# Performance work log

Hardware: AMD Instinct MI355X
Metric: run time of the kernel (lower is better)

Reference implementation:

```python
import jax, jax.numpy as jnp
from jax import lax
import numpy as np


def conv2d(x, w, b=None, stride=1, pad=0, groups=1):
    out = lax.conv_general_dilated(x, w, (stride, stride), [(pad, pad), (pad, pad)],
                                   dimension_numbers=('NCHW', 'OIHW', 'NCHW'),
                                   feature_group_count=groups)
    if b is not None:
        out = out + b[None, :, None, None]
    return out


def ln(x, g, b, eps=1e-5):
    m = x.mean(-1, keepdims=True)
    v = ((x - m) ** 2).mean(-1, keepdims=True)
    return (x - m) * lax.rsqrt(v + eps) * g + b


def grid_sample_bilinear(img, grid):
    # img [N,C,H,W]; grid [N,Hg,Wg,2] with (x,y) in [-1,1]; align_corners=True, zeros padding
    N, C, H, W = img.shape
    x = (grid[..., 0] + 1.0) * 0.5 * (W - 1)
    y = (grid[..., 1] + 1.0) * 0.5 * (H - 1)
    x0 = jnp.floor(x); y0 = jnp.floor(y)
    x1 = x0 + 1.0; y1 = y0 + 1.0
    wx1 = x - x0; wx0 = 1.0 - wx1
    wy1 = y - y0; wy0 = 1.0 - wy1
    imgh = img.transpose(0, 2, 3, 1)  # [N,H,W,C]
    bidx = jnp.arange(N)[:, None, None]
    def g(ix, iy):
        valid = (ix >= 0) & (ix <= W - 1) & (iy >= 0) & (iy <= H - 1)
        ixc = jnp.clip(ix, 0, W - 1).astype(jnp.int32)
        iyc = jnp.clip(iy, 0, H - 1).astype(jnp.int32)
        return imgh[bidx, iyc, ixc] * valid[..., None].astype(img.dtype)
    out = (g(x0, y0) * (wx0 * wy0)[..., None] + g(x1, y0) * (wx1 * wy0)[..., None]
           + g(x0, y1) * (wx0 * wy1)[..., None] + g(x1, y1) * (wx1 * wy1)[..., None])
    return out.transpose(0, 3, 1, 2)  # [N,C,Hg,Wg]


def setup_inputs() -> dict:
    key = jax.random.key(0)
    ks = iter(jax.random.split(key, 64))
    def rn(shape, s=0.02):
        return jax.random.normal(next(ks), shape, jnp.float32) * s
    B, C, H, W = 4, 512, 32, 32
    gc, hid = 256, 1024
    d = {}
    d['feat_tgt'] = jax.random.normal(next(ks), (B, C, H, W), jnp.float32)
    d['feat_ref'] = jax.random.normal(next(ks), (B, C, H, W), jnp.float32)
    d['emb_w'] = rn((C, 2 * C, 3, 3)); d['emb_b'] = jnp.zeros((C,), jnp.float32)
    d['q_w'] = rn((C, C)); d['q_b'] = jnp.zeros((C,), jnp.float32)
    d['k_w'] = rn((C, C)); d['k_b'] = jnp.zeros((C,), jnp.float32)
    d['v_w'] = rn((C, C)); d['v_b'] = jnp.zeros((C,), jnp.float32)
    d['out_w'] = rn((C, C)); d['out_b'] = jnp.zeros((C,), jnp.float32)
    d['ln1_w'] = jnp.ones((gc,), jnp.float32); d['ln1_b'] = jnp.zeros((gc,), jnp.float32)
    d['mb_n1_w'] = jnp.ones((gc,), jnp.float32); d['mb_n1_b'] = jnp.zeros((gc,), jnp.float32)
    d['mb_q_w'] = rn((gc, gc)); d['mb_q_b'] = jnp.zeros((gc,), jnp.float32)
    d['mb_kv_w'] = rn((2 * gc, gc)); d['mb_kv_b'] = jnp.zeros((2 * gc,), jnp.float32)
    d['mb_proj_w'] = rn((gc, gc)); d['mb_proj_b'] = jnp.zeros((gc,), jnp.float32)
    d['mb_n2_w'] = jnp.ones((gc,), jnp.float32); d['mb_n2_b'] = jnp.zeros((gc,), jnp.float32)
    d['mb_fc1_w'] = rn((hid, gc)); d['mb_fc1_b'] = jnp.zeros((hid,), jnp.float32)
    d['mb_dw_w'] = rn((hid, 1, 3, 3)); d['mb_dw_b'] = jnp.zeros((hid,), jnp.float32)
    d['mb_fc2_w'] = rn((gc, hid)); d['mb_fc2_b'] = jnp.zeros((gc,), jnp.float32)
    d['co_dw_w'] = rn((gc, 1, 9, 9)); d['co_dw_b'] = jnp.zeros((gc,), jnp.float32)
    d['co_ln_w'] = jnp.ones((gc,), jnp.float32); d['co_ln_b'] = jnp.zeros((gc,), jnp.float32)
    d['co_out_w'] = rn((2, gc))
    return d


def reference(feat_tgt, feat_ref, emb_w, emb_b, q_w, q_b, k_w, k_b, v_w, v_b, out_w, out_b,
              ln1_w, ln1_b, mb_n1_w, mb_n1_b, mb_q_w, mb_q_b, mb_kv_w, mb_kv_b,
              mb_proj_w, mb_proj_b, mb_n2_w, mb_n2_b, mb_fc1_w, mb_fc1_b, mb_dw_w, mb_dw_b,
              mb_fc2_w, mb_fc2_b, co_dw_w, co_dw_b, co_ln_w, co_ln_b, co_out_w):
    B, C, H, W = feat_tgt.shape
    G = 2                      # n_groups
    gc = C // G                # n_group_channels
    heads, hc = 8, C // 8      # n_heads, n_head_channels
    # embedding conv over concat(target, reference)
    feat = conv2d(jnp.concatenate([feat_tgt, feat_ref], 1), emb_w, emb_b, pad=1)
    q = jnp.einsum('bchw,oc->bohw', feat_tgt, q_w) + q_b[None, :, None, None]
    # group tokens + LN
    fg = feat.reshape(B * G, gc, H * W).transpose(0, 2, 1)  # [BG, N, gc]
    x = ln(fg, ln1_w, ln1_b)
    # ---- MitBlock offset generator ----
    BG, N, D = x.shape
    mh = 8; mhd = D // mh
    h = ln(x, mb_n1_w, mb_n1_b, 1e-6)
    qq = (h @ mb_q_w.T + mb_q_b).reshape(BG, N, mh, mhd).transpose(0, 2, 1, 3)
    kv = (h @ mb_kv_w.T + mb_kv_b).reshape(BG, N, 2, mh, mhd).transpose(2, 0, 3, 1, 4)
    kk, vv = kv[0], kv[1]
    a = jax.nn.softmax(jnp.einsum('bhnd,bhmd->bhnm', qq, kk) * (mhd ** -0.5), axis=-1)
    o = jnp.einsum('bhnm,bhmd->bhnd', a, vv).transpose(0, 2, 1, 3).reshape(BG, N, D)
    x = x + (o @ mb_proj_w.T + mb_proj_b)
    h2 = ln(x, mb_n2_w, mb_n2_b, 1e-6)
    m = h2 @ mb_fc1_w.T + mb_fc1_b                         # [BG, N, hid]
    hid = m.shape[-1]
    mi = m.transpose(0, 2, 1).reshape(BG, hid, H, W)
    mi = conv2d(mi, mb_dw_w, mb_dw_b, pad=1, groups=hid)
    m = jax.nn.gelu(mi.reshape(BG, hid, N).transpose(0, 2, 1), approximate=False)
    x = x + (m @ mb_fc2_w.T + mb_fc2_b)
    # ---- conv_offset stack ----
    off = x.reshape(BG, H, W, gc).transpose(0, 3, 1, 2)
    off = conv2d(off, co_dw_w, co_dw_b, pad=4, groups=gc)
    off = ln(off.transpose(0, 2, 3, 1), co_ln_w, co_ln_b).transpose(0, 3, 1, 2)
    off = jax.nn.gelu(off, approximate=False)
    off = jnp.einsum('bchw,oc->bohw', off, co_out_w)       # [BG, 2, Hk, Wk]
    Hk, Wk = off.shape[2], off.shape[3]
    ns = Hk * Wk
    rng = jnp.array([1.0 / Hk, 1.0 / Wk], feat.dtype).reshape(1, 2, 1, 1)
    off = jnp.tanh(off) * rng * 2.0                        # offset_range_factor = 2
    off = off.transpose(0, 2, 3, 1)                        # [BG, Hk, Wk, 2] (y,x)
    ry = (jnp.linspace(0.5, Hk - 0.5, Hk, dtype=feat.dtype) / Hk) * 2 - 1
    rx = (jnp.linspace(0.5, Wk - 0.5, Wk, dtype=feat.dtype) / Wk) * 2 - 1
    ref = jnp.stack(jnp.meshgrid(ry, rx, indexing='ij'), -1)  # [Hk, Wk, 2] (y,x)
    pos = off + ref[None]
    sampled = grid_sample_bilinear(feat.reshape(BG, gc, H, W), pos[..., ::-1])
    sampled = sampled.reshape(B, C, ns)
    k = jnp.einsum('bcn,oc->bon', sampled, k_w) + k_b[None, :, None]
    v = jnp.einsum('bcn,oc->bon', sampled, v_w) + v_b[None, :, None]
    qh = q.reshape(B * heads, hc, H * W)
    kh = k.reshape(B * heads, hc, ns)
    vh = v.reshape(B * heads, hc, ns)
    attn = jax.nn.softmax(jnp.einsum('bcm,bcn->bmn', qh, kh) * (hc ** -0.5), axis=-1)
    out = jnp.einsum('bmn,bcn->bcm', attn, vh).reshape(B, C, H, W)
    y = jnp.einsum('bchw,oc->bohw', out, out_w) + out_b[None, :, None, None]
    return y
```

## Files before the change

### kernel.cpp

```cpp
#include <hip/hip_runtime.h>
#include <math.h>


static constexpr int HW = 1024;

typedef __attribute__((ext_vector_type(8))) short bf16x8;
typedef __attribute__((ext_vector_type(4))) float f32x4;

union V16u { int4 i4; ushort u[8]; };

__device__ __forceinline__ float gelu_exact(float v) {
  return 0.5f * v * (1.0f + erff(v * 0.7071067811865475f));
}

__device__ __forceinline__ ushort bf16_rne(float v) {
  unsigned int b = __float_as_uint(v);
  return (ushort)((b + 0x7fffu + ((b >> 16) & 1u)) >> 16);
}

__device__ __forceinline__ void split2(float v, ushort& h, ushort& l) {
  h = bf16_rne(v);
  l = bf16_rne(v - __uint_as_float(((unsigned int)h) << 16));
}

__global__ void k_prepw(const float* __restrict__ w, ushort* __restrict__ Wt_hi,
                        ushort* __restrict__ Wt_lo) {
  int idx = blockIdx.x * 256 + threadIdx.x;
  int o = idx >> 10, ci = idx & 1023;
  const float* src = w + (size_t)idx * 9;
#pragma unroll
  for (int t = 0; t < 9; ++t) {
    ushort h, l; split2(src[t], h, l);
    size_t oo = ((size_t)(t * 512 + o)) * 1024 + ci;
    Wt_hi[oo] = h; Wt_lo[oo] = l;
  }
}

__global__ void k_prepx(const float* __restrict__ tgt, const float* __restrict__ refp,
                        ushort* __restrict__ Xt_hi, ushort* __restrict__ Xt_lo) {
  int idx = blockIdx.x * 256 + threadIdx.x;
  int xp = idx % 34; int r = idx / 34;
  int g8 = r & 127; r >>= 7;
  int yp = r % 34; int b = r / 34;
  int y = yp - 1, x = xp - 1;
  bool valid = (unsigned)y < 32u && (unsigned)x < 32u;
  V16u hi, lo;
  const float* in = (g8 < 64) ? (tgt + ((size_t)(b * 512 + g8 * 8)) * HW)
                              : (refp + ((size_t)(b * 512 + (g8 - 64) * 8)) * HW);
#pragma unroll
  for (int j = 0; j < 8; ++j) {
    float v = valid ? in[(size_t)j * HW + y * 32 + x] : 0.f;
    split2(v, hi.u[j], lo.u[j]);
  }
  size_t oo = (((size_t)(b * 34 + yp)) * 34 + xp) * 1024 + g8 * 8;
  *(int4*)(Xt_hi + oo) = hi.i4;
  *(int4*)(Xt_lo + oo) = lo.i4;
}

__global__ __launch_bounds__(256, 2)
void k_emb_mfma(const ushort* __restrict__ Xt_hi, const ushort* __restrict__ Xt_lo,
                const ushort* __restrict__ Wt_hi, const ushort* __restrict__ Wt_lo,
                float* __restrict__ part) {
  int wgid = (blockIdx.x & 7) * 64 + (blockIdx.x >> 3);
  int yt = wgid & 7;  wgid >>= 3;
  int b  = wgid & 3;  wgid >>= 2;
  int mt = wgid & 3;  wgid >>= 2;
  int ks = wgid;
  int tid = threadIdx.x;
  int w = tid >> 6, l = tid & 63;
  int lr = l & 15, lu = l >> 4;
  int y0 = yt * 4;
  int obase = mt * 128 + w * 32;

  __shared__ int4 LsH[2][816];
  __shared__ int4 LsL[2][816];

  int4 gh[4], gl[4];
  int kc0 = ks * 8;

  auto loadstage = [&](int kcg) {
#pragma unroll
    for (int i = 0; i < 4; ++i) {
      int s = tid + 256 * i;
      if (s < 816) {
        int px = s >> 2;
        int u = (s & 3) ^ ((px >> 1) & 3);
        size_t off = ((size_t)(b * 34 + y0) * 34 + px) * 1024 + kcg * 32 + u * 8;
        gh[i] = *(const int4*)(Xt_hi + off);
        gl[i] = *(const int4*)(Xt_lo + off);
// ... 65 lines not shown
  for (int a = 0; a < 2; ++a)
#pragma unroll
    for (int yr = 0; yr < 4; ++yr)
#pragma unroll
      for (int h = 0; h < 2; ++h) {
        f32x4 c = acc[a][yr * 2 + h];
        size_t base = ((size_t)(b * 512 + obase + a * 16 + lu * 4)) * 1024
                      + (y0 + yr) * 32 + h * 16 + lr;
#pragma unroll
        for (int r = 0; r < 4; ++r) pb[base + (size_t)r * 1024] = c[r];
      }
}

__global__ void k_embmerge_nc(const float* __restrict__ part, const float* __restrict__ bias,
                              float* __restrict__ featnc) {
  __shared__ float T[64][65];
  int bid = blockIdx.x;
  int n0 = (bid & 15) << 6; bid >>= 4;
  int c0 = (bid & 3) << 6; int bg = bid >> 2;
  int cl = threadIdx.x & 63, rw = threadIdx.x >> 6;
#pragma unroll
  for (int i = 0; i < 16; ++i) {
    int crow = i * 4 + rw;
    size_t idx = ((size_t)(bg * 256 + c0 + crow)) * 1024 + n0 + cl;
    float v = part[idx] + part[2097152 + idx] + part[4194304 + idx] + part[6291456 + idx];
    T[crow][cl] = v + bias[(bg & 1) * 256 + c0 + crow];
  }
  __syncthreads();
#pragma unroll
  for (int i = 0; i < 16; ++i) {
    int nrow = i * 4 + rw;
    featnc[((size_t)(bg * 1024 + n0 + nrow)) * 256 + c0 + cl] = T[cl][nrow];
  }
}

__device__ __forceinline__ void wfrag_body(const float* __restrict__ W, int K, int KC,
                                           ushort* __restrict__ dh, ushort* __restrict__ dl,
                                           int gtid) {
  int l = gtid & 63; int fr = gtid >> 6;
  int kc = fr % KC; int ot = fr / KC;
  int lr = l & 15, lu = l >> 4;
  const float* sp = W + (size_t)(ot * 16 + lr) * K + kc * 32 + lu * 8;
  V16u hi, lo;
#pragma unroll
  for (int j = 0; j < 8; ++j) split2(sp[j], hi.u[j], lo.u[j]);
  *(int4*)(dh + (size_t)gtid * 8) = hi.i4;
  *(int4*)(dl + (size_t)gtid * 8) = lo.i4;
}

__global__ void k_prep_wfrag9(
    const float* q_w, const float* k_w, const float* v_w, const float* o_w,
    const float* mq_w, const float* mkv_w, const float* mp_w,
    const float* f1_w, const float* f2_w, const float* dw9_w,
    ushort* qh, ushort* ql, ushort* kh, ushort* kl, ushort* vh, ushort* vl,
    ushort* oh, ushort* ol, ushort* mqh, ushort* mql, ushort* mkvh, ushort* mkvl,
    ushort* mph, ushort* mpl, ushort* f1h, ushort* f1l, ushort* f2h, ushort* f2l,
    float* wt9) {
  int bid = blockIdx.x, tid = threadIdx.x;
  if (bid < 128)      wfrag_body(q_w, 512, 16, qh, ql, bid * 256 + tid);
  else if (bid < 256) wfrag_body(k_w, 512, 16, kh, kl, (bid - 128) * 256 + tid);
  else if (bid < 384) wfrag_body(v_w, 512, 16, vh, vl, (bid - 256) * 256 + tid);
  else if (bid < 512) wfrag_body(o_w, 512, 16, oh, ol, (bid - 384) * 256 + tid);
  else if (bid < 544) wfrag_body(mq_w, 256, 8, mqh, mql, (bid - 512) * 256 + tid);
  else if (bid < 608) wfrag_body(mkv_w, 256, 8, mkvh, mkvl, (bid - 544) * 256 + tid);
  else if (bid < 640) wfrag_body(mp_w, 256, 8, mph, mpl, (bid - 608) * 256 + tid);
  else if (bid < 768) wfrag_body(f1_w, 256, 8, f1h, f1l, (bid - 640) * 256 + tid);
  else if (bid < 896) wfrag_body(f2_w, 1024, 32, f2h, f2l, (bid - 768) * 256 + tid);
  else {
    int idx = (bid - 896) * 256 + tid;
    int t = idx >> 8, c = idx & 255;
    wt9[idx] = dw9_w[c * 81 + t];
  }
}

__global__ void k_prep_cm2frag(const float* __restrict__ src, int CH, int KC,
                               ushort* __restrict__ dh, ushort* __restrict__ dl) {
  int gtid = blockIdx.x * 256 + threadIdx.x;
  int l = gtid & 63; int fr = gtid >> 6;
  int kc = fr % KC; int r2 = fr / KC; int nt = r2 & 63; int b = r2 >> 6;
  int lr = l & 15, lu = l >> 4;
  const float* sp = src + ((size_t)(b * CH) + kc * 32 + lu * 8) * 1024 + nt * 16 + lr;
  V16u hi, lo;
#pragma unroll
  for (int j = 0; j < 8; ++j) split2(sp[(size_t)j * 1024], hi.u[j], lo.u[j]);
  *(int4*)(dh + (size_t)gtid * 8) = hi.i4;
  *(int4*)(dl + (size_t)gtid * 8) = lo.i4;
}

__global__ void k_prep_s2frag(const float* __restrict__ snc,
                              ushort* __restrict__ dh, ushort* __restrict__ dl) {
  int gtid = blockIdx.x * 256 + threadIdx.x;
  int l = gtid & 63; int fr = gtid >> 6;
  int kc = fr & 15; int nt = (fr >> 4) & 63; int b = fr >> 10;
  int lr = l & 15, lu = l >> 4;
  const float* sp = snc + ((size_t)((b * 2 + (kc >> 3)) * 1024 + nt * 16 + lr)) * 256
                    + (kc & 7) * 32 + lu * 8;
  V16u hi, lo;
#pragma unroll
  for (int j = 0; j < 8; ++j) split2(sp[j], hi.u[j], lo.u[j]);
  *(int4*)(dh + (size_t)gtid * 8) = hi.i4;
  *(int4*)(dl + (size_t)gtid * 8) = lo.i4;
}

__global__ __launch_bounds__(256)
void k_gemm_mfma(const ushort* __restrict__ Ah, const ushort* __restrict__ Al,
                 const ushort* __restrict__ Bh, const ushort* __restrict__ Bl,
                 const float* __restrict__ bias, float* __restrict__ Y,
                 int KC, int MT, int Mtot) {
  int bid = blockIdx.x;
  int ntb = bid & 15; bid >>= 4;
  int mt = bid % MT; int b = bid / MT;
  int tid = threadIdx.x, w = tid >> 6, l = tid & 63, lr = l & 15, lu = l >> 4;
  int wo = w >> 1, wn = w & 1;
  int ot0 = mt * 4 + wo * 2;
  int nf0 = ntb * 4 + wn * 2;
  const bf16x8* pAh = (const bf16x8*)Ah;
  const bf16x8* pAl = (const bf16x8*)Al;
  const bf16x8* pBh = (const bf16x8*)Bh;
  const bf16x8* pBl = (const bf16x8*)Bl;
// ... 43 lines not shown
#pragma unroll
  for (int i = 0; i < 16; ++i) {
    int crow = i * 4 + rw;
    T[crow][cl] = Pcm[((size_t)(bg * 256 + c0 + crow)) * 1024 + n0 + cl];
  }
  __syncthreads();
#pragma unroll
  for (int i = 0; i < 16; ++i) {
    int nrow = i * 4 + rw;
    Xtm[((size_t)((bg << 10) + n0 + nrow)) * 256 + c0 + cl] += T[cl][nrow];
  }
}

__global__ void k_transadd_nc(const float* __restrict__ Yg, const float* __restrict__ Xtm,
                              float* __restrict__ out_nc) {
  __shared__ float T[64][65];
  int bid = blockIdx.x; int n0 = (bid & 15) << 6; bid >>= 4;
  int c0 = (bid & 3) << 6; int bg = bid >> 2;
  int cl = threadIdx.x & 63, rw = threadIdx.x >> 6;
#pragma unroll
  for (int i = 0; i < 16; ++i) {
    int crow = i * 4 + rw;
    T[crow][cl] = Yg[((size_t)(bg * 256 + c0 + crow)) * 1024 + n0 + cl];
  }
  __syncthreads();
#pragma unroll
  for (int i = 0; i < 16; ++i) {
    int nrow = i * 4 + rw;
    size_t a = ((size_t)((bg << 10) + n0 + nrow)) * 256 + c0 + cl;
    out_nc[a] = T[cl][nrow] + Xtm[a];
  }
}

__global__ void k_ln_tok(const float* __restrict__ xin, const float* __restrict__ g_,
                         const float* __restrict__ b_, float* __restrict__ yo, float eps) {
  int token = (blockIdx.x * 256 + threadIdx.x) >> 6;
  int lane = threadIdx.x & 63;
  float4 v4 = *reinterpret_cast<const float4*>(xin + (size_t)token * 256 + lane * 4);
  float s  = v4.x + v4.y + v4.z + v4.w;
  float s2 = v4.x * v4.x + v4.y * v4.y + v4.z * v4.z + v4.w * v4.w;
#pragma unroll
  for (int off = 32; off; off >>= 1) { s += __shfl_xor(s, off); s2 += __shfl_xor(s2, off); }
  float mean = s * (1.f / 256.f);
  float rstd = rsqrtf(s2 * (1.f / 256.f) - mean * mean + eps);
  float4 g4 = *reinterpret_cast<const float4*>(g_ + lane * 4);
  float4 b4 = *reinterpret_cast<const float4*>(b_ + lane * 4);
  float4 o;
  o.x = (v4.x - mean) * rstd * g4.x + b4.x;
  o.y = (v4.y - mean) * rstd * g4.y + b4.y;
  o.z = (v4.z - mean) * rstd * g4.z + b4.z;
  o.w = (v4.w - mean) * rstd * g4.w + b4.w;
  *reinterpret_cast<float4*>(yo + (size_t)token * 256 + lane * 4) = o;
}

__global__ void k_ln_frag(const float* __restrict__ xin, const float* __restrict__ g_,
                          const float* __restrict__ b_, ushort* __restrict__ dh,
                          ushort* __restrict__ dl, float eps) {
  int token = (blockIdx.x * 256 + threadIdx.x) >> 6;
  int lane = threadIdx.x & 63;
  float4 v4 = *reinterpret_cast<const float4*>(xin + (size_t)token * 256 + lane * 4);
  float s  = v4.x + v4.y + v4.z + v4.w;
  float s2 = v4.x * v4.x + v4.y * v4.y + v4.z * v4.z + v4.w * v4.w;
#pragma unroll
  for (int off = 32; off; off >>= 1) { s += __shfl_xor(s, off); s2 += __shfl_xor(s2, off); }
  float mean = s * (1.f / 256.f);
  float rstd = rsqrtf(s2 * (1.f / 256.f) - mean * mean + eps);
  float4 g4 = *reinterpret_cast<const float4*>(g_ + lane * 4);
  float4 b4 = *reinterpret_cast<const float4*>(b_ + lane * 4);
  float vals[4];
  vals[0] = (v4.x - mean) * rstd * g4.x + b4.x;
  vals[1] = (v4.y - mean) * rstd * g4.y + b4.y;
  vals[2] = (v4.z - mean) * rstd * g4.z + b4.z;
  vals[3] = (v4.w - mean) * rstd * g4.w + b4.w;
  ushort4 h4, l4;
  split2(vals[0], h4.x, l4.x); split2(vals[1], h4.y, l4.y);
  split2(vals[2], h4.z, l4.z); split2(vals[3], h4.w, l4.w);
  int bg = token >> 10, nt = (token >> 4) & 63, lr = token & 15;
  int kc = lane >> 3, lu_f = (lane >> 1) & 3, j0 = (lane & 1) * 4;
  size_t base = ((((size_t)(bg * 64 + nt)) * 8 + kc) * 64 + lu_f * 16 + lr) * 8 + j0;
  *(ushort4*)(dh + base) = h4;
  *(ushort4*)(dl + base) = l4;
}

__global__ void k_prep_mb3(const float* __restrict__ qq_cm, const float* __restrict__ kv_cm,
                           ushort* __restrict__ mQh, ushort* __restrict__ mQl,
                           ushort* __restrict__ mKh, ushort* __restrict__ mKl,
                           ushort* __restrict__ mVh, ushort* __restrict__ mVl) {
  int bid = blockIdx.x, tid = threadIdx.x;
  int sect = bid >> 10, lb = bid & 1023;
  int gtid = lb * 256 + tid;
  int l = gtid & 63; int fr = gtid >> 6;
  int lr = l & 15, lu = l >> 4;
  V16u hi, lo;
  if (sect < 2) {
    int nt = fr & 63; int bgh = fr >> 6;
    int bg = bgh >> 3, hh = bgh & 7;
    const float* src = sect == 0 ? qq_cm : kv_cm;
    int CH = sect == 0 ? 256 : 512;
    float scale = sect == 0 ? 0.17677669529663689f : 1.f;
    const float* sp = src + ((size_t)(bg * CH + hh * 32 + lu * 8)) * 1024 + nt * 16 + lr;
#pragma unroll
    for (int j = 0; j < 8; ++j) split2(sp[(size_t)j * 1024] * scale, hi.u[j], lo.u[j]);
    ushort* dh = sect == 0 ? mQh : mKh;
    ushort* dl = sect == 0 ? mQl : mKl;
    *(int4*)(dh + (size_t)gtid * 8) = hi.i4;
    *(int4*)(dl + (size_t)gtid * 8) = lo.i4;
  } else {
    int kc = fr & 31; int et = (fr >> 5) & 1; int bgh = fr >> 6;
    int bg = bgh >> 3, hh = bgh & 7;
    const float* sp = kv_cm + ((size_t)(bg * 512 + 256 + hh * 32 + et * 16 + lr)) * 1024
                      + kc * 32 + lu * 8;
#pragma unroll
    for (int j = 0; j < 8; ++j) split2(sp[j], hi.u[j], lo.u[j]);
    *(int4*)(mVh + (size_t)gtid * 8) = hi.i4;
    *(int4*)(mVl + (size_t)gtid * 8) = lo.i4;
  }
}

__global__ void k_prep_main3(const float* __restrict__ qb, const float* __restrict__ kb,
                             const float* __restrict__ vb,
                             ushort* __restrict__ aQh, ushort* __restrict__ aQl,
                             ushort* __restrict__ aKh, ushort* __restrict__ aKl,
                             ushort* __restrict__ aVh, ushort* __restrict__ aVl) {
  int bid = blockIdx.x, tid = threadIdx.x;
  int sect = bid >> 10, lb = bid & 1023;
  int gtid = lb * 256 + tid;
  int l = gtid & 63, tile = gtid >> 6;
  int lr = l & 15, lu = l >> 4;
  V16u hi, lo;
  if (sect < 2) {
    int dc = tile & 1, nt = (tile >> 1) & 63, bh = tile >> 7;
    int b = bh >> 3, h = bh & 7;
    const float* src = sect == 0 ? qb : kb;
    float scale = sect == 0 ? 0.125f : 1.f;
    const float* sp = src + ((size_t)(b * 512 + h * 64 + dc * 32 + lu * 8)) * 1024
                      + nt * 16 + lr;
#pragma unroll
    for (int j = 0; j < 8; ++j) split2(sp[(size_t)j * 1024] * scale, hi.u[j], lo.u[j]);
    ushort* dh = sect == 0 ? aQh : aKh;
    ushort* dl = sect == 0 ? aQl : aKl;
    *(int4*)(dh + (size_t)gtid * 8) = hi.i4;
    *(int4*)(dl + (size_t)gtid * 8) = lo.i4;
  } else {
    int kc = tile & 31, et = (tile >> 5) & 3, bh = tile >> 7;
    int b = bh >> 3, h = bh & 7;
    const float* sp = vb + ((size_t)(b * 512 + h * 64 + et * 16 + lr)) * 1024 + kc * 32 + lu * 8;
#pragma unroll
    for (int j = 0; j < 8; ++j) split2(sp[j], hi.u[j], lo.u[j]);
    *(int4*)(aVh + (size_t)gtid * 8) = hi.i4;
    *(int4*)(aVl + (size_t)gtid * 8) = lo.i4;
  }
}

__global__ __launch_bounds__(256)
void k_mbattn_mfma(const ushort* __restrict__ Qh, const ushort* __restrict__ Ql,
                   const ushort* __restrict__ Kh, const ushort* __restrict__ Kl,
                   const ushort* __restrict__ Vh, const ushort* __restrict__ Vl,
                   ushort* __restrict__ ofh, ushort* __restrict__ ofl) {
  int qb = blockIdx.x & 15, bgh = blockIdx.x >> 4;
  int tid = threadIdx.x, w = tid >> 6, l = tid & 63, lr = l & 15, lu = l >> 4;
  int qt = qb * 4 + w;
  bf16x8 qh = ((const bf16x8*)Qh)[(size_t)(bgh * 64 + qt) * 64 + l];
  bf16x8 ql = ((const bf16x8*)Ql)[(size_t)(bgh * 64 + qt) * 64 + l];
  __shared__ ushort Ph[4][16][72];
  __shared__ ushort Pl[4][16][72];
  f32x4 zero = {0.f, 0.f, 0.f, 0.f};
  f32x4 oacc[2] = {zero, zero};
  float den = 0.f;
  for (int kb = 0; kb < 16; ++kb) {
#pragma unroll
    for (int kt4 = 0; kt4 < 4; ++kt4) {
      int kt = kb * 4 + kt4;
      bf16x8 kh = ((const bf16x8*)Kh)[(size_t)(bgh * 64 + kt) * 64 + l];
      bf16x8 kl = ((const bf16x8*)Kl)[(size_t)(bgh * 64 + kt) * 64 + l];
      f32x4 s = zero;
      s = __builtin_amdgcn_mfma_f32_16x16x32_bf16(kh, qh, s, 0, 0, 0);
      s = __builtin_amdgcn_mfma_f32_16x16x32_bf16(kh, ql, s, 0, 0, 0);
      s = __builtin_amdgcn_mfma_f32_16x16x32_bf16(kl, qh, s, 0, 0, 0);
      uint2 uh, ul;
// ... 265 lines not shown
  const float* n1_b   = (const float*)d_in[15];
  const float* mbq_w  = (const float*)d_in[16];
  const float* mbq_b  = (const float*)d_in[17];
  const float* mbkv_w = (const float*)d_in[18];
  const float* mbkv_b = (const float*)d_in[19];
  const float* mbp_w  = (const float*)d_in[20];
  const float* mbp_b  = (const float*)d_in[21];
  const float* n2_w   = (const float*)d_in[22];
  const float* n2_b   = (const float*)d_in[23];
  const float* fc1_w  = (const float*)d_in[24];
  const float* fc1_b  = (const float*)d_in[25];
  const float* dw3_w  = (const float*)d_in[26];
  const float* dw3_b  = (const float*)d_in[27];
  const float* fc2_w  = (const float*)d_in[28];
  const float* fc2_b  = (const float*)d_in[29];
  const float* dw9_w  = (const float*)d_in[30];
  const float* dw9_b  = (const float*)d_in[31];
  const float* coln_w = (const float*)d_in[32];
  const float* coln_b = (const float*)d_in[33];
  const float* coout_w= (const float*)d_in[34];

  float* ws = (float*)d_ws;
  float* slabA = ws + 0;
  float* qbuf  = ws + 2097152;
  float* xbuf  = ws + 4194304;
  float* slabD = ws + 6291456;
  float* slabE = ws + 8388608;
  float* slabF = ws + 10485760;
  float* slabG = ws + 14680064;
  float* slabH = ws + 23068672;
  float* featnc= ws + 31457280;
  float* posb  = ws + 35389440;
  float* wt9   = ws + 35405824;

  ushort* XtH = (ushort*)(ws + 4194304);
  ushort* XtL = XtH + 4734976;
  ushort* WtEH = (ushort*)slabG;
  ushort* WtEL = WtEH + 4718592;
  float* part = slabH;
  ushort* tgtfh = (ushort*)slabF;
  ushort* tgtfl = tgtfh + 2097152;

  ushort* J = (ushort*)(ws + 33554432);
  ushort* wfq_h = J;                ushort* wfq_l = J + 262144;
  ushort* wfk_h = J + 524288;       ushort* wfk_l = J + 786432;
  ushort* wfv_h = J + 1048576;      ushort* wfv_l = J + 1310720;
  ushort* wfo_h = J + 1572864;      ushort* wfo_l = J + 1835008;
  ushort* wfmq_h = J + 2097152;     ushort* wfmq_l = J + 2162688;
  ushort* wfmkv_h = J + 2228224;    ushort* wfmkv_l = J + 2359296;
  ushort* wfmp_h = J + 2490368;     ushort* wfmp_l = J + 2555904;
  ushort* wff1_h = J + 2621440;     ushort* wff1_l = J + 2883584;
  ushort* wff2_h = J + 3145728;     ushort* wff2_l = J + 3407872;

  ushort* hfh = (ushort*)slabG;     ushort* hfl = hfh + 2097152;
  float* qq_cm  = slabE;
  float* kv_cm  = slabF;
  ushort* mQh = (ushort*)slabG;     ushort* mQl = mQh + 2097152;
  ushort* mKh = mQh + 4194304;      ushort* mKl = mQh + 6291456;
  ushort* mVh = mQh + 8388608;      ushort* mVl = mQh + 10485760;
  ushort* ofh = (ushort*)slabF;     ushort* ofl = ofh + 2097152;
  float* P_cm = slabD;
  ushort* h2fh = (ushort*)slabF;    ushort* h2fl = h2fh + 2097152;
  float* m_cm = slabG;
  float* mi_cm = slabH;
  ushort* mifh = (ushort*)slabG;    ushort* mifl = mifh + 8388608;
  float* ygemm = slabD;
  float* offin = slabA;
  float* offdwnc = slabE;
  float* samplednc = slabA;
  ushort* sfh = (ushort*)slabF;     ushort* sfl = sfh + 2097152;
  float* kbuf = slabD;
  float* vbuf = slabE;
  ushort* aQh = (ushort*)slabG;     ushort* aQl = aQh + 2097152;
  ushort* aKh = aQh + 4194304;      ushort* aKl = aQh + 6291456;
  ushort* aVh = aQh + 8388608;      ushort* aVl = aQh + 10485760;
  ushort* anfh = (ushort*)slabH;    ushort* anfl = anfh + 2097152;

  k_prepw<<<2048, 256, 0, stream>>>(emb_w, WtEH, WtEL);
  k_prepx<<<2312, 256, 0, stream>>>(tgt, refp, XtH, XtL);
  k_prep_wfrag9<<<977, 256, 0, stream>>>(q_w, k_w, v_w, out_w, mbq_w, mbkv_w, mbp_w,
                                         fc1_w, fc2_w, dw9_w,
                                         wfq_h, wfq_l, wfk_h, wfk_l, wfv_h, wfv_l,
                                         wfo_h, wfo_l, wfmq_h, wfmq_l, wfmkv_h, wfmkv_l,
                                         wfmp_h, wfmp_l, wff1_h, wff1_l, wff2_h, wff2_l,
                                         wt9);
  k_prep_cm2frag<<<1024, 256, 0, stream>>>(tgt, 512, 16, tgtfh, tgtfl);
  k_emb_mfma<<<512, 256, 0, stream>>>(XtH, XtL, WtEH, WtEL, part);
  k_embmerge_nc<<<512, 256, 0, stream>>>(part, emb_b, featnc);
  k_gemm_mfma<<<512, 256, 0, stream>>>(wfq_h, wfq_l, tgtfh, tgtfl, q_b, qbuf, 16, 8, 512);
  k_ln_tok<<<2048, 256, 0, stream>>>(featnc, ln1_w, ln1_b, xbuf, 1e-5f);
  k_ln_frag<<<2048, 256, 0, stream>>>(xbuf, n1_w, n1_b, hfh, hfl, 1e-6f);
  k_gemm_mfma<<<512, 256, 0, stream>>>(wfmq_h, wfmq_l, hfh, hfl, mbq_b, qq_cm, 8, 4, 256);
  k_gemm_mfma<<<1024, 256, 0, stream>>>(wfmkv_h, wfmkv_l, hfh, hfl, mbkv_b, kv_cm, 8, 8, 512);
  k_prep_mb3<<<3072, 256, 0, stream>>>(qq_cm, kv_cm, mQh, mQl, mKh, mKl, mVh, mVl);
  k_mbattn_mfma<<<1024, 256, 0, stream>>>(mQh, mQl, mKh, mKl, mVh, mVl, ofh, ofl);
  k_gemm_mfma<<<512, 256, 0, stream>>>(wfmp_h, wfmp_l, ofh, ofl, mbp_b, P_cm, 8, 4, 256);
  k_transadd_tm<<<512, 256, 0, stream>>>(P_cm, xbuf);
  k_ln_frag<<<2048, 256, 0, stream>>>(xbuf, n2_w, n2_b, h2fh, h2fl, 1e-6f);
  k_gemm_mfma<<<2048, 256, 0, stream>>>(wff1_h, wff1_l, h2fh, h2fl, fc1_b, m_cm, 8, 16, 1024);
  k_dw3<<<32768, 256, 0, stream>>>(m_cm, dw3_w, dw3_b, mi_cm);
  k_prep_cm2frag<<<4096, 256, 0, stream>>>(mi_cm, 1024, 32, mifh, mifl);
  k_gemm_mfma<<<512, 256, 0, stream>>>(wff2_h, wff2_l, mifh, mifl, fc2_b, ygemm, 32, 4, 256);
  k_transadd_nc<<<512, 256, 0, stream>>>(ygemm, xbuf, offin);
  k_dw9_nc<<<1024, 256, 0, stream>>>(offin, wt9, dw9_b, offdwnc);
  k_cotail_nc<<<2048, 256, 0, stream>>>(offdwnc, coln_w, coln_b, coout_w, posb);
  k_gsample_nc<<<128, 256, 0, stream>>>(featnc, posb, samplednc);
  k_prep_s2frag<<<1024, 256, 0, stream>>>(samplednc, sfh, sfl);
  k_gemm_mfma<<<512, 256, 0, stream>>>(wfk_h, wfk_l, sfh, sfl, k_b, kbuf, 16, 8, 512);
  k_gemm_mfma<<<512, 256, 0, stream>>>(wfv_h, wfv_l, sfh, sfl, v_b, vbuf, 16, 8, 512);
  k_prep_main3<<<3072, 256, 0, stream>>>(qbuf, kbuf, vbuf, aQh, aQl, aKh, aKl, aVh, aVl);
  k_mainattn_mfma<<<512, 256, 0, stream>>>(aQh, aQl, aKh, aKl, aVh, aVl, anfh, anfl);
  k_gemm_mfma<<<512, 256, 0, stream>>>(wfo_h, wfo_l, anfh, anfl, out_b, (float*)d_out, 16, 8, 512);
}
```

Measured before the change: 619.2 us.

## Merge prep kernels, fuse both layernorms, and concatenate QKV and KV projection GEMMs

Folds the three weight/input prep launches into one kernel, which also concatenates biases. Fuses LN1 and the n1 norm into one kernel that writes both the fp32 token buffer and the bf16 hi/lo fragments. Merges the separate q/kv projections (mixer) and k/v projections (main attention) into single wider GEMMs over concatenated weights. The aim is fewer launches and fewer passes over the activation inputs, at the cost of new buffer layouts whose offsets must stay consistent.

Result: faster. 591.5 us (-4.5%).

```diff
diff --git a/kernel.cpp b/kernel.cpp
--- a/kernel.cpp
+++ b/kernel.cpp
@@ -23,38 +23,100 @@
   l = bf16_rne(v - __uint_as_float(((unsigned int)h) << 16));
 }
 
-__global__ void k_prepw(const float* __restrict__ w, ushort* __restrict__ Wt_hi,
-                        ushort* __restrict__ Wt_lo) {
-  int idx = blockIdx.x * 256 + threadIdx.x;
-  int o = idx >> 10, ci = idx & 1023;
-  const float* src = w + (size_t)idx * 9;
-#pragma unroll
-  for (int t = 0; t < 9; ++t) {
-    ushort h, l; split2(src[t], h, l);
-    size_t oo = ((size_t)(t * 512 + o)) * 1024 + ci;
-    Wt_hi[oo] = h; Wt_lo[oo] = l;
-  }
-}
-
-__global__ void k_prepx(const float* __restrict__ tgt, const float* __restrict__ refp,
-                        ushort* __restrict__ Xt_hi, ushort* __restrict__ Xt_lo) {
-  int idx = blockIdx.x * 256 + threadIdx.x;
-  int xp = idx % 34; int r = idx / 34;
-  int g8 = r & 127; r >>= 7;
-  int yp = r % 34; int b = r / 34;
-  int y = yp - 1, x = xp - 1;
-  bool valid = (unsigned)y < 32u && (unsigned)x < 32u;
+__device__ __forceinline__ void wfrag_body(const float* __restrict__ W, int K, int KC,
+                                           ushort* __restrict__ dh, ushort* __restrict__ dl,
+                                           int gtid) {
+  int l = gtid & 63; int fr = gtid >> 6;
+  int kc = fr % KC; int ot = fr / KC;
+  int lr = l & 15, lu = l >> 4;
+  const float* sp = W + (size_t)(ot * 16 + lr) * K + kc * 32 + lu * 8;
   V16u hi, lo;
-  const float* in = (g8 < 64) ? (tgt + ((size_t)(b * 512 + g8 * 8)) * HW)
-                              : (refp + ((size_t)(b * 512 + (g8 - 64) * 8)) * HW);
-#pragma unroll
-  for (int j = 0; j < 8; ++j) {
-    float v = valid ? in[(size_t)j * HW + y * 32 + x] : 0.f;
-    split2(v, hi.u[j], lo.u[j]);
-  }
-  size_t oo = (((size_t)(b * 34 + yp)) * 34 + xp) * 1024 + g8 * 8;
-  *(int4*)(Xt_hi + oo) = hi.i4;
-  *(int4*)(Xt_lo + oo) = lo.i4;
+#pragma unroll
+  for (int j = 0; j < 8; ++j) split2(sp[j], hi.u[j], lo.u[j]);
+  *(int4*)(dh + (size_t)gtid * 8) = hi.i4;
+  *(int4*)(dl + (size_t)gtid * 8) = lo.i4;
+}
+
+__global__ void k_prep_all(
+    const float* __restrict__ emb_w, const float* __restrict__ tgt,
+    const float* __restrict__ refp,
+    const float* q_w, const float* k_w, const float* v_w, const float* o_w,
+    const float* mq_w, const float* mkv_w, const float* mp_w,
+    const float* f1_w, const float* f2_w, const float* dw9_w,
+    const float* mq_b, const float* mkv_b, const float* k_b, const float* v_b,
+    ushort* __restrict__ WtEH, ushort* __restrict__ WtEL,
+    ushort* __restrict__ XtH, ushort* __restrict__ XtL,
+    ushort* qh, ushort* ql, ushort* kvh, ushort* kvl,
+    ushort* oh, ushort* ol, ushort* mqkvh, ushort* mqkvl,
+    ushort* mph, ushort* mpl, ushort* f1h, ushort* f1l, ushort* f2h, ushort* f2l,
+    float* wt9, float* biasmb, float* biaskv) {
+  int bid = blockIdx.x, tid = threadIdx.x;
+  if (bid < 2048) {
+    int idx = bid * 256 + tid;
+    int o = idx >> 10, ci = idx & 1023;
+    const float* src = emb_w + (size_t)idx * 9;
+#pragma unroll
+    for (int t = 0; t < 9; ++t) {
+      ushort h, l; split2(src[t], h, l);
+      size_t oo = ((size_t)(t * 512 + o)) * 1024 + ci;
+      WtEH[oo] = h; WtEL[oo] = l;
+    }
+  } else if (bid < 4360) {
+    int idx = (bid - 2048) * 256 + tid;
+    int xp = idx % 34; int r = idx / 34;
+    int g8 = r & 127; r >>= 7;
+    int yp = r % 34; int b = r / 34;
+    int y = yp - 1, x = xp - 1;
+    bool valid = (unsigned)y < 32u && (unsigned)x < 32u;
+    V16u hi, lo;
+    const float* in = (g8 < 64) ? (tgt + ((size_t)(b * 512 + g8 * 8)) * HW)
+                                : (refp + ((size_t)(b * 512 + (g8 - 64) * 8)) * HW);
+#pragma unroll
+    for (int j = 0; j < 8; ++j) {
+      float v = valid ? in[(size_t)j * HW + y * 32 + x] : 0.f;
+      split2(v, hi.u[j], lo.u[j]);
+    }
+    size_t oo = (((size_t)(b * 34 + yp)) * 34 + xp) * 1024 + g8 * 8;
+    *(int4*)(XtH + oo) = hi.i4;
+    *(int4*)(XtL + oo) = lo.i4;
+  }
+  else if (bid < 4488) wfrag_body(q_w, 512, 16, qh, ql, (bid - 4360) * 256 + tid);
+  else if (bid < 4616) wfrag_body(k_w, 512, 16, kvh, kvl, (bid - 4488) * 256 + tid);
+  else if (bid < 4744) wfrag_body(v_w, 512, 16, kvh + 262144, kvl + 262144,
+                                  (bid - 4616) * 256 + tid);
+  else if (bid < 4872) wfrag_body(o_w, 512, 16, oh, ol, (bid - 4744) * 256 + tid);
+  else if (bid < 4904) wfrag_body(mq_w, 256, 8, mqkvh, mqkvl, (bid - 4872) * 256 + tid);
+  else if (bid < 4968) wfrag_body(mkv_w, 256, 8, mqkvh + 65536, mqkvl + 65536,
+                                  (bid - 4904) * 256 + tid);
+  else if (bid < 5000) wfrag_body(mp_w, 256, 8, mph, mpl, (bid - 4968) * 256 + tid);
+  else if (bid < 5128) wfrag_body(f1_w, 256, 8, f1h, f1l, (bid - 5000) * 256 + tid);
+  else if (bid < 5256) wfrag_body(f2_w, 1024, 32, f2h, f2l, (bid - 5128) * 256 + tid);
+  else if (bid < 5337) {
+    int idx = (bid - 5256) * 256 + tid;
+    int t = idx >> 8, c = idx & 255;
+    wt9[idx] = dw9_w[c * 81 + t];
+  } else {
+    int idx = (bid - 5337) * 256 + tid;
+    if (idx < 768) biasmb[idx] = idx < 256 ? mq_b[idx] : mkv_b[idx - 256];
+    else if (idx < 1792) {
+      int j = idx - 768;
+      biaskv[j] = j < 512 ? k_b[j] : v_b[j - 512];
+    }
+  }
+}
+
+__global__ void k_prep_cm2frag(const float* __restrict__ src, int CH, int KC,
+                               ushort* __restrict__ dh, ushort* __restrict__ dl) {
+  int gtid = blockIdx.x * 256 + threadIdx.x;
+  int l = gtid & 63; int fr = gtid >> 6;
+  int kc = fr % KC; int r2 = fr / KC; int nt = r2 & 63; int b = r2 >> 6;
+  int lr = l & 15, lu = l >> 4;
+  const float* sp = src + ((size_t)(b * CH) + kc * 32 + lu * 8) * 1024 + nt * 16 + lr;
+  V16u hi, lo;
+#pragma unroll
+  for (int j = 0; j < 8; ++j) split2(sp[(size_t)j * 1024], hi.u[j], lo.u[j]);
+  *(int4*)(dh + (size_t)gtid * 8) = hi.i4;
+  *(int4*)(dl + (size_t)gtid * 8) = lo.i4;
 }
 
 __global__ __launch_bounds__(256, 2)
@@ -186,59 +248,6 @@
     int nrow = i * 4 + rw;
     featnc[((size_t)(bg * 1024 + n0 + nrow)) * 256 + c0 + cl] = T[cl][nrow];
   }
-}
-
-__device__ __forceinline__ void wfrag_body(const float* __restrict__ W, int K, int KC,
-                                           ushort* __restrict__ dh, ushort* __restrict__ dl,
-                                           int gtid) {
-  int l = gtid & 63; int fr = gtid >> 6;
-  int kc = fr % KC; int ot = fr / KC;
-  int lr = l & 15, lu = l >> 4;
-  const float* sp = W + (size_t)(ot * 16 + lr) * K + kc * 32 + lu * 8;
-  V16u hi, lo;
-#pragma unroll
-  for (int j = 0; j < 8; ++j) split2(sp[j], hi.u[j], lo.u[j]);
-  *(int4*)(dh + (size_t)gtid * 8) = hi.i4;
-  *(int4*)(dl + (size_t)gtid * 8) = lo.i4;
-}
-
-__global__ void k_prep_wfrag9(
-    const float* q_w, const float* k_w, const float* v_w, const float* o_w,
-    const float* mq_w, const float* mkv_w, const float* mp_w,
-    const float* f1_w, const float* f2_w, const float* dw9_w,
-    ushort* qh, ushort* ql, ushort* kh, ushort* kl, ushort* vh, ushort* vl,
-    ushort* oh, ushort* ol, ushort* mqh, ushort* mql, ushort* mkvh, ushort* mkvl,
-    ushort* mph, ushort* mpl, ushort* f1h, ushort* f1l, ushort* f2h, ushort* f2l,
-    float* wt9) {
-  int bid = blockIdx.x, tid = threadIdx.x;
-  if (bid < 128)      wfrag_body(q_w, 512, 16, qh, ql, bid * 256 + tid);
-  else if (bid < 256) wfrag_body(k_w, 512, 16, kh, kl, (bid - 128) * 256 + tid);
-  else if (bid < 384) wfrag_body(v_w, 512, 16, vh, vl, (bid - 256) * 256 + tid);
-  else if (bid < 512) wfrag_body(o_w, 512, 16, oh, ol, (bid - 384) * 256 + tid);
-  else if (bid < 544) wfrag_body(mq_w, 256, 8, mqh, mql, (bid - 512) * 256 + tid);
-  else if (bid < 608) wfrag_body(mkv_w, 256, 8, mkvh, mkvl, (bid - 544) * 256 + tid);
-  else if (bid < 640) wfrag_body(mp_w, 256, 8, mph, mpl, (bid - 608) * 256 + tid);
-  else if (bid < 768) wfrag_body(f1_w, 256, 8, f1h, f1l, (bid - 640) * 256 + tid);
-  else if (bid < 896) wfrag_body(f2_w, 1024, 32, f2h, f2l, (bid - 768) * 256 + tid);
-  else {
-    int idx = (bid - 896) * 256 + tid;
-    int t = idx >> 8, c = idx & 255;
-    wt9[idx] = dw9_w[c * 81 + t];
-  }
-}
-
-__global__ void k_prep_cm2frag(const float* __restrict__ src, int CH, int KC,
-                               ushort* __restrict__ dh, ushort* __restrict__ dl) {
-  int gtid = blockIdx.x * 256 + threadIdx.x;
-  int l = gtid & 63; int fr = gtid >> 6;
-  int kc = fr % KC; int r2 = fr / KC; int nt = r2 & 63; int b = r2 >> 6;
-  int lr = l & 15, lu = l >> 4;
-  const float* sp = src + ((size_t)(b * CH) + kc * 32 + lu * 8) * 1024 + nt * 16 + lr;
-  V16u hi, lo;
-#pragma unroll
-  for (int j = 0; j < 8; ++j) split2(sp[(size_t)j * 1024], hi.u[j], lo.u[j]);
-  *(int4*)(dh + (size_t)gtid * 8) = hi.i4;
-  *(int4*)(dl + (size_t)gtid * 8) = lo.i4;
 }
 
 __global__ void k_prep_s2frag(const float* __restrict__ snc,
@@ -348,25 +357,46 @@
   }
 }
 
-__global__ void k_ln_tok(const float* __restrict__ xin, const float* __restrict__ g_,
-                         const float* __restrict__ b_, float* __restrict__ yo, float eps) {
+__global__ void k_ln1n1(const float* __restrict__ featnc,
+                        const float* __restrict__ g1, const float* __restrict__ b1,
+                        const float* __restrict__ gn, const float* __restrict__ bn,
+                        float* __restrict__ xbuf,
+                        ushort* __restrict__ dh, ushort* __restrict__ dl) {
   int token = (blockIdx.x * 256 + threadIdx.x) >> 6;
   int lane = threadIdx.x & 63;
-  float4 v4 = *reinterpret_cast<const float4*>(xin + (size_t)token * 256 + lane * 4);
+  float4 v4 = *reinterpret_cast<const float4*>(featnc + (size_t)token * 256 + lane * 4);
   float s  = v4.x + v4.y + v4.z + v4.w;
   float s2 = v4.x * v4.x + v4.y * v4.y + v4.z * v4.z + v4.w * v4.w;
 #pragma unroll
   for (int off = 32; off; off >>= 1) { s += __shfl_xor(s, off); s2 += __shfl_xor(s2, off); }
   float mean = s * (1.f / 256.f);
-  float rstd = rsqrtf(s2 * (1.f / 256.f) - mean * mean + eps);
-  float4 g4 = *reinterpret_cast<const float4*>(g_ + lane * 4);
-  float4 b4 = *reinterpret_cast<const float4*>(b_ + lane * 4);
-  float4 o;
-  o.x = (v4.x - mean) * rstd * g4.x + b4.x;
-  o.y = (v4.y - mean) * rstd * g4.y + b4.y;
-  o.z = (v4.z - mean) * rstd * g4.z + b4.z;
-  o.w = (v4.w - mean) * rstd * g4.w + b4.w;
-  *reinterpret_cast<float4*>(yo + (size_t)token * 256 + lane * 4) = o;
+  float rstd = rsqrtf(s2 * (1.f / 256.f) - mean * mean + 1e-5f);
+  float4 g4 = *reinterpret_cast<const float4*>(g1 + lane * 4);
+  float4 b4 = *reinterpret_cast<const float4*>(b1 + lane * 4);
+  float4 x;
+  x.x = (v4.x - mean) * rstd * g4.x + b4.x;
+  x.y = (v4.y - mean) * rstd * g4.y + b4.y;
+  x.z = (v4.z - mean) * rstd * g4.z + b4.z;
+  x.w = (v4.w - mean) * rstd * g4.w + b4.w;
+  *reinterpret_cast<float4*>(xbuf + (size_t)token * 256 + lane * 4) = x;
+  float t  = x.x + x.y + x.z + x.w;
+  float t2 = x.x * x.x + x.y * x.y + x.z * x.z + x.w * x.w;
+#pragma unroll
+  for (int off = 32; off; off >>= 1) { t += __shfl_xor(t, off); t2 += __shfl_xor(t2, off); }
+  float mean2 = t * (1.f / 256.f);
+  float rstd2 = rsqrtf(t2 * (1.f / 256.f) - mean2 * mean2 + 1e-6f);
+  float4 gg = *reinterpret_cast<const float4*>(gn + lane * 4);
+  float4 bb = *reinterpret_cast<const float4*>(bn + lane * 4);
+  ushort4 h4, l4;
+  split2((x.x - mean2) * rstd2 * gg.x + bb.x, h4.x, l4.x);
+  split2((x.y - mean2) * rstd2 * gg.y + bb.y, h4.y, l4.y);
+  split2((x.z - mean2) * rstd2 * gg.z + bb.z, h4.z, l4.z);
+  split2((x.w - mean2) * rstd2 * gg.w + bb.w, h4.w, l4.w);
+  int bg = token >> 10, nt = (token >> 4) & 63, lr = token & 15;
+  int kc = lane >> 3, lu_f = (lane >> 1) & 3, j0 = (lane & 1) * 4;
+  size_t base = ((((size_t)(bg * 64 + nt)) * 8 + kc) * 64 + lu_f * 16 + lr) * 8 + j0;
+  *(ushort4*)(dh + base) = h4;
+  *(ushort4*)(dl + base) = l4;
 }
 
 __global__ void k_ln_frag(const float* __restrict__ xin, const float* __restrict__ g_,
@@ -383,14 +413,11 @@
   float rstd = rsqrtf(s2 * (1.f / 256.f) - mean * mean + eps);
   float4 g4 = *reinterpret_cast<const float4*>(g_ + lane * 4);
   float4 b4 = *reinterpret_cast<const float4*>(b_ + lane * 4);
-  float vals[4];
-  vals[0] = (v4.x - mean) * rstd * g4.x + b4.x;
-  vals[1] = (v4.y - mean) * rstd * g4.y + b4.y;
-  vals[2] = (v4.z - mean) * rstd * g4.z + b4.z;
-  vals[3] = (v4.w - mean) * rstd * g4.w + b4.w;
   ushort4 h4, l4;
-  split2(vals[0], h4.x, l4.x); split2(vals[1], h4.y, l4.y);
-  split2(vals[2], h4.z, l4.z); split2(vals[3], h4.w, l4.w);
+  split2((v4.x - mean) * rstd * g4.x + b4.x, h4.x, l4.x);
+  split2((v4.y - mean) * rstd * g4.y + b4.y, h4.y, l4.y);
+  split2((v4.z - mean) * rstd * g4.z + b4.z, h4.z, l4.z);
+  split2((v4.w - mean) * rstd * g4.w + b4.w, h4.w, l4.w);
   int bg = token >> 10, nt = (token >> 4) & 63, lr = token & 15;
   int kc = lane >> 3, lu_f = (lane >> 1) & 3, j0 = (lane & 1) * 4;
   size_t base = ((((size_t)(bg * 64 + nt)) * 8 + kc) * 64 + lu_f * 16 + lr) * 8 + j0;
@@ -398,7 +425,7 @@
   *(ushort4*)(dl + base) = l4;
 }
 
-__global__ void k_prep_mb3(const float* __restrict__ qq_cm, const float* __restrict__ kv_cm,
+__global__ void k_prep_mb3(const float* __restrict__ qkv,
                            ushort* __restrict__ mQh, ushort* __restrict__ mQl,
                            ushort* __restrict__ mKh, ushort* __restrict__ mKl,
                            ushort* __restrict__ mVh, ushort* __restrict__ mVl) {
@@ -411,10 +438,10 @@
   if (sect < 2) {
     int nt = fr & 63; int bgh = fr >> 6;
     int bg = bgh >> 3, hh = bgh & 7;
-    const float* src = sect == 0 ? qq_cm : kv_cm;
-    int CH = sect == 0 ? 256 : 512;
+    int rowbase = sect == 0 ? 0 : 256;
     float scale = sect == 0 ? 0.17677669529663689f : 1.f;
-    const float* sp = src + ((size_t)(bg * CH + hh * 32 + lu * 8)) * 1024 + nt * 16 + lr;
+    const float* sp = qkv + ((size_t)(bg * 768 + rowbase + hh * 32 + lu * 8)) * 1024
+                      + nt * 16 + lr;
 #pragma unroll
     for (int j = 0; j < 8; ++j) split2(sp[(size_t)j * 1024] * scale, hi.u[j], lo.u[j]);
     ushort* dh = sect == 0 ? mQh : mKh;
@@ -424,7 +451,7 @@
   } else {
     int kc = fr & 31; int et = (fr >> 5) & 1; int bgh = fr >> 6;
     int bg = bgh >> 3, hh = bgh & 7;
-    const float* sp = kv_cm + ((size_t)(bg * 512 + 256 + hh * 32 + et * 16 + lr)) * 1024
+    const float* sp = qkv + ((size_t)(bg * 768 + 512 + hh * 32 + et * 16 + lr)) * 1024
                       + kc * 32 + lu * 8;
 #pragma unroll
     for (int j = 0; j < 8; ++j) split2(sp[j], hi.u[j], lo.u[j]);
@@ -433,8 +460,7 @@
   }
 }
 
-__global__ void k_prep_main3(const float* __restrict__ qb, const float* __restrict__ kb,
-                             const float* __restrict__ vb,
+__global__ void k_prep_main3(const float* __restrict__ qb, const float* __restrict__ kv2,
                              ushort* __restrict__ aQh, ushort* __restrict__ aQl,
                              ushort* __restrict__ aKh, ushort* __restrict__ aKl,
                              ushort* __restrict__ aVh, ushort* __restrict__ aVl) {
@@ -447,10 +473,15 @@
   if (sect < 2) {
     int dc = tile & 1, nt = (tile >> 1) & 63, bh = tile >> 7;
     int b = bh >> 3, h = bh & 7;
-    const float* src = sect == 0 ? qb : kb;
-    float scale = sect == 0 ? 0.125f : 1.f;
-    const float* sp = src + ((size_t)(b * 512 + h * 64 + dc * 32 + lu * 8)) * 1024
-                      + nt * 16 + lr;
+    const float* sp;
+    float scale;
+    if (sect == 0) {
+      scale = 0.125f;
+      sp = qb + ((size_t)(b * 512 + h * 64 + dc * 32 + lu * 8)) * 1024 + nt * 16 + lr;
+    } else {
+      scale = 1.f;
+      sp = kv2 + ((size_t)(b * 1024 + h * 64 + dc * 32 + lu * 8)) * 1024 + nt * 16 + lr;
+    }
 #pragma unroll
     for (int j = 0; j < 8; ++j) split2(sp[(size_t)j * 1024] * scale, hi.u[j], lo.u[j]);
     ushort* dh = sect == 0 ? aQh : aKh;
@@ -460,7 +491,8 @@
   } else {
     int kc = tile & 31, et = (tile >> 5) & 3, bh = tile >> 7;
     int b = bh >> 3, h = bh & 7;
-    const float* sp = vb + ((size_t)(b * 512 + h * 64 + et * 16 + lr)) * 1024 + kc * 32 + lu * 8;
+    const float* sp = kv2 + ((size_t)(b * 1024 + 512 + h * 64 + et * 16 + lr)) * 1024
+                      + kc * 32 + lu * 8;
 #pragma unroll
     for (int j = 0; j < 8; ++j) split2(sp[j], hi.u[j], lo.u[j]);
     *(int4*)(aVh + (size_t)gtid * 8) = hi.i4;
@@ -792,6 +824,8 @@
   float* featnc= ws + 31457280;
   float* posb  = ws + 35389440;
   float* wt9   = ws + 35405824;
+  float* biasmb= ws + 35426560;
+  float* biaskv= ws + 35427328;
 
   ushort* XtH = (ushort*)(ws + 4194304);
   ushort* XtL = XtH + 4734976;
@@ -802,19 +836,16 @@
   ushort* tgtfl = tgtfh + 2097152;
 
   ushort* J = (ushort*)(ws + 33554432);
-  ushort* wfq_h = J;                ushort* wfq_l = J + 262144;
-  ushort* wfk_h = J + 524288;       ushort* wfk_l = J + 786432;
-  ushort* wfv_h = J + 1048576;      ushort* wfv_l = J + 1310720;
-  ushort* wfo_h = J + 1572864;      ushort* wfo_l = J + 1835008;
-  ushort* wfmq_h = J + 2097152;     ushort* wfmq_l = J + 2162688;
-  ushort* wfmkv_h = J + 2228224;    ushort* wfmkv_l = J + 2359296;
-  ushort* wfmp_h = J + 2490368;     ushort* wfmp_l = J + 2555904;
-  ushort* wff1_h = J + 2621440;     ushort* wff1_l = J + 2883584;
-  ushort* wff2_h = J + 3145728;     ushort* wff2_l = J + 3407872;
+  ushort* wfq_h   = J;                ushort* wfq_l   = J + 262144;
+  ushort* wfkv_h  = J + 524288;       ushort* wfkv_l  = J + 1048576;
+  ushort* wfo_h   = J + 1572864;      ushort* wfo_l   = J + 1835008;
+  ushort* wfmqkv_h= J + 2097152;      ushort* wfmqkv_l= J + 2293760;
+  ushort* wfmp_h  = J + 2490368;      ushort* wfmp_l  = J + 2555904;
+  ushort* wff1_h  = J + 2621440;      ushort* wff1_l  = J + 2883584;
+  ushort* wff2_h  = J + 3145728;      ushort* wff2_l  = J + 3407872;
 
   ushort* hfh = (ushort*)slabG;     ushort* hfl = hfh + 2097152;
-  float* qq_cm  = slabE;
-  float* kv_cm  = slabF;
+  float* qkv_cm = slabE;
   ushort* mQh = (ushort*)slabG;     ushort* mQl = mQh + 2097152;
   ushort* mKh = mQh + 4194304;      ushort* mKl = mQh + 6291456;
   ushort* mVh = mQh + 8388608;      ushort* mVl = mQh + 10485760;
@@ -829,30 +860,26 @@
   float* offdwnc = slabE;
   float* samplednc = slabA;
   ushort* sfh = (ushort*)slabF;     ushort* sfl = sfh + 2097152;
-  float* kbuf = slabD;
-  float* vbuf = slabE;
+  float* kv2 = slabD;
   ushort* aQh = (ushort*)slabG;     ushort* aQl = aQh + 2097152;
   ushort* aKh = aQh + 4194304;      ushort* aKl = aQh + 6291456;
   ushort* aVh = aQh + 8388608;      ushort* aVl = aQh + 10485760;
   ushort* anfh = (ushort*)slabH;    ushort* anfl = anfh + 2097152;
 
-  k_prepw<<<2048, 256, 0, stream>>>(emb_w, WtEH, WtEL);
-  k_prepx<<<2312, 256, 0, stream>>>(tgt, refp, XtH, XtL);
-  k_prep_wfrag9<<<977, 256, 0, stream>>>(q_w, k_w, v_w, out_w, mbq_w, mbkv_w, mbp_w,
-                                         fc1_w, fc2_w, dw9_w,
-                                         wfq_h, wfq_l, wfk_h, wfk_l, wfv_h, wfv_l,
-                                         wfo_h, wfo_l, wfmq_h, wfmq_l, wfmkv_h, wfmkv_l,
-                                         wfmp_h, wfmp_l, wff1_h, wff1_l, wff2_h, wff2_l,
-                                         wt9);
+  k_prep_all<<<5344, 256, 0, stream>>>(
+      emb_w, tgt, refp, q_w, k_w, v_w, out_w, mbq_w, mbkv_w, mbp_w, fc1_w, fc2_w,
+      dw9_w, mbq_b, mbkv_b, k_b, v_b,
+      WtEH, WtEL, XtH, XtL,
+      wfq_h, wfq_l, wfkv_h, wfkv_l, wfo_h, wfo_l, wfmqkv_h, wfmqkv_l,
+      wfmp_h, wfmp_l, wff1_h, wff1_l, wff2_h, wff2_l,
+      wt9, biasmb, biaskv);
   k_prep_cm2frag<<<1024, 256, 0, stream>>>(tgt, 512, 16, tgtfh, tgtfl);
   k_emb_mfma<<<512, 256, 0, stream>>>(XtH, XtL, WtEH, WtEL, part);
   k_embmerge_nc<<<512, 256, 0, stream>>>(part, emb_b, featnc);
   k_gemm_mfma<<<512, 256, 0, stream>>>(wfq_h, wfq_l, tgtfh, tgtfl, q_b, qbuf, 16, 8, 512);
-  k_ln_tok<<<2048, 256, 0, stream>>>(featnc, ln1_w, ln1_b, xbuf, 1e-5f);
-  k_ln_frag<<<2048, 256, 0, stream>>>(xbuf, n1_w, n1_b, hfh, hfl, 1e-6f);
-  k_gemm_mfma<<<512, 256, 0, stream>>>(wfmq_h, wfmq_l, hfh, hfl, mbq_b, qq_cm, 8, 4, 256);
-  k_gemm_mfma<<<1024, 256, 0, stream>>>(wfmkv_h, wfmkv_l, hfh, hfl, mbkv_b, kv_cm, 8, 8, 512);
-  k_prep_mb3<<<3072, 256, 0, stream>>>(qq_cm, kv_cm, mQh, mQl, mKh, mKl, mVh, mVl);
+  k_ln1n1<<<2048, 256, 0, stream>>>(featnc, ln1_w, ln1_b, n1_w, n1_b, xbuf, hfh, hfl);
+  k_gemm_mfma<<<1536, 256, 0, stream>>>(wfmqkv_h, wfmqkv_l, hfh, hfl, biasmb, qkv_cm, 8, 12, 768);
+  k_prep_mb3<<<3072, 256, 0, stream>>>(qkv_cm, mQh, mQl, mKh, mKl, mVh, mVl);
   k_mbattn_mfma<<<1024, 256, 0, stream>>>(mQh, mQl, mKh, mKl, mVh, mVl, ofh, ofl);
   k_gemm_mfma<<<512, 256, 0, stream>>>(wfmp_h, wfmp_l, ofh, ofl, mbp_b, P_cm, 8, 4, 256);
   k_transadd_tm<<<512, 256, 0, stream>>>(P_cm, xbuf);
@@ -866,9 +893,8 @@
   k_cotail_nc<<<2048, 256, 0, stream>>>(offdwnc, coln_w, coln_b, coout_w, posb);
   k_gsample_nc<<<128, 256, 0, stream>>>(featnc, posb, samplednc);
   k_prep_s2frag<<<1024, 256, 0, stream>>>(samplednc, sfh, sfl);
-  k_gemm_mfma<<<512, 256, 0, stream>>>(wfk_h, wfk_l, sfh, sfl, k_b, kbuf, 16, 8, 512);
-  k_gemm_mfma<<<512, 256, 0, stream>>>(wfv_h, wfv_l, sfh, sfl, v_b, vbuf, 16, 8, 512);
-  k_prep_main3<<<3072, 256, 0, stream>>>(qbuf, kbuf, vbuf, aQh, aQl, aKh, aKl, aVh, aVl);
+  k_gemm_mfma<<<1024, 256, 0, stream>>>(wfkv_h, wfkv_l, sfh, sfl, biaskv, kv2, 16, 16, 1024);
+  k_prep_main3<<<3072, 256, 0, stream>>>(qbuf, kv2, aQh, aQl, aKh, aKl, aVh, aVl);
   k_mainattn_mfma<<<512, 256, 0, stream>>>(aQh, aQl, aKh, aKl, aVh, aVl, anfh, anfl);
   k_gemm_mfma<<<512, 256, 0, stream>>>(wfo_h, wfo_l, anfh, anfl, out_b, (float*)d_out, 16, 8, 512);
 }
```
